# Kernel optimization log

Hardware: AMD Instinct MI355X
Metric: run time of the kernel (lower is better)

Reference implementation:

```python
import jax, jax.numpy as jnp
import numpy as np

B, CIN, COUT = 4, 256, 256
H, W = 48, 48
KH = KW = 7
SH = SW = 1
PH = PW = 3
REL = COUT // 2  # rel_size with groups=1


def setup_inputs() -> dict:
    key = jax.random.key(0)
    ks = jax.random.split(key, 7)
    fan = float(CIN)
    x = jax.random.normal(ks[0], (B, CIN, H, W), jnp.float32)
    w_q = jax.random.normal(ks[1], (COUT, CIN), jnp.float32) * (2.0 / fan) ** 0.5
    w_k = jax.random.normal(ks[2], (COUT, CIN), jnp.float32) * (2.0 / fan) ** 0.5
    w_v = jax.random.normal(ks[3], (COUT, CIN), jnp.float32) * (2.0 / fan) ** 0.5
    bound = 1.0 / np.sqrt(COUT)
    bias = jax.random.uniform(ks[4], (1, COUT, 1, 1), jnp.float32, -bound, bound)
    rel_x = jax.random.normal(ks[5], (REL, KW), jnp.float32)
    rel_y = jax.random.normal(ks[6], (COUT - REL, KH), jnp.float32)
    return {"x": x, "w_q": w_q, "w_k": w_k, "w_v": w_v, "bias": bias,
            "rel_x": rel_x, "rel_y": rel_y}


def reference(x, w_q, w_k, w_v, bias, rel_x, rel_y):
    b = x.shape[0]
    ph, pw = H + 2 * PH, W + 2 * PW
    fh = (ph - KH) // SH + 1
    fw = (pw - KW) // SW + 1
    xp = jnp.pad(x, ((0, 0), (0, 0), (PH, PH), (PW, PW)))
    # 1x1 convs (groups=1) as channel matmuls
    vq = jnp.einsum('oc,bchw->bohw', w_q, xp)
    vk = jnp.einsum('oc,bchw->bohw', w_k, xp)
    vv = jnp.einsum('oc,bchw->bohw', w_v, xp)
    # query at window centers: [b, C, fh, fw]
    win_q = vq[:, :, (KH - 1) // 2: ph - KH // 2: SH, (KW - 1) // 2: pw - KW // 2: SW]
    # relative position terms (sum over channel halves)
    qx = jnp.einsum('bxhw,xk->bhwk', win_q[:, :REL], rel_x)        # [b,fh,fw,kw]
    qy = jnp.einsum('byhw,yk->bhwk', win_q[:, REL:], rel_y)        # [b,fh,fw,kh]
    # overlapping windows via gather (equivalent to torch unfold)
    I = jnp.arange(fh)[:, None] * SH + jnp.arange(KH)[None, :]     # [fh,kh]
    J = jnp.arange(fw)[:, None] * SW + jnp.arange(KW)[None, :]     # [fw,kw]
    win_k = vk[:, :, I[:, None, :, None], J[None, :, None, :]]     # [b,C,fh,fw,kh,kw]
    # channel-summed attention logits (shared across channels, as in source)
    scores = jnp.einsum('bchw,bchwkl->bhwkl', win_q, win_k)
    scores = scores + qy[:, :, :, :, None] + qx[:, :, :, None, :]
    attn = jax.nn.softmax(scores.reshape(b, fh, fw, KH * KW), axis=-1)
    attn = attn.reshape(b, fh, fw, KH, KW)
    win_v = vv[:, :, I[:, None, :, None], J[None, :, None, :]]     # [b,C,fh,fw,kh,kw]
    out = jnp.einsum('bhwkl,bchwkl->bchw', attn, win_v) + bias
    return out
```

## Files before the change

### kernel.cpp

```cpp
#include <hip/hip_runtime.h>

#define BB 4
#define CC 256
#define HH 48
#define WW 48
#define HWHW 2304
#define KK 49
#define RELN 128

#define QSZ (BB*CC*HWHW)
#define ATTNOFF (3*QSZ)
#define SBUF_FLOATS (BB*HH*64*WW)
#define WTOFF (ATTNOFF + SBUF_FLOATS)
#define WT_FLOATS 196608
#define KBOFF (WTOFF + WT_FLOATS)
#define KB_FLOATS 3145728
#define RBOFF (KBOFF + KB_FLOATS)

typedef short bf16x8 __attribute__((ext_vector_type(8)));
typedef float f32x4 __attribute__((ext_vector_type(4)));

__device__ __forceinline__ void split_bf16(float f, unsigned short& hi, unsigned short& lo)
{
    unsigned u = __float_as_uint(f);
    hi = (unsigned short)(u >> 16);
    float r = f - __uint_as_float(u & 0xFFFF0000u);
    unsigned v = __float_as_uint(r);
    v += 0x7FFFu + ((v >> 16) & 1u);
    lo = (unsigned short)(v >> 16);
}

__device__ __forceinline__ void gload16(const uint4* g, uint4* l)
{
    __builtin_amdgcn_global_load_lds(
        (const __attribute__((address_space(1))) void*)g,
        (__attribute__((address_space(3))) void*)l, 16, 0, 0);
}

__global__ __launch_bounds__(256) void prep_kernel(
    const float* __restrict__ x,
    const float* __restrict__ wq, const float* __restrict__ wk,
    const float* __restrict__ wvp,
    const float* __restrict__ relx, const float* __restrict__ rely,
    unsigned short* __restrict__ xt, unsigned short* __restrict__ wt,
    float* __restrict__ ws)
{
    __shared__ unsigned short lds[32*520];
    const int bid = blockIdx.x;
    const int t = threadIdx.x;

    if (bid < 288) {
        const int b = bid / 72;
        const int hw0 = (bid % 72) * 32;
        const int hw = t & 31, cp = t >> 5;
        #pragma unroll 4
        for (int i = 0; i < 32; ++i) {
            int c = i*8 + cp;
            float f = x[((size_t)b*CC + c)*HWHW + hw0 + hw];
            unsigned short hi, lo; split_bf16(f, hi, lo);
            int ch = i*2;
            lds[hw*520 + ((ch       ^ (hw&7))*8) + cp] = hi;
            lds[hw*520 + (((ch + 1) ^ (hw&7))*8) + cp] = lo;
        }
        __syncthreads();
        const int hw2 = t >> 3, u = t & 7;
        uint4* xt4 = (uint4*)xt;
        const size_t rowbase = ((size_t)b*HWHW + hw0 + hw2) * 64;
        #pragma unroll
        for (int j = 0; j < 8; ++j) {
            int chunk = j*8 + u;
            uint4 v = *(const uint4*)&lds[hw2*520 + chunk*8];
            xt4[rowbase + chunk] = v;
        }
        return;
    }
    if (bid < 384) {
        const int tt = (bid - 288)*256 + t;
        const int m = tt >> 5, kg = tt & 31;
        const float* src = (m < 256) ? wq : (m < 512) ? wk : wvp;
        const float* row = src + (size_t)(m & 255)*256 + kg*8;
        unsigned short h[8], l[8];
        #pragma unroll
        for (int j = 0; j < 8; ++j) split_bf16(row[j], h[j], l[j]);
        uint4 hv, lv;
        hv.x = (unsigned)h[0] | ((unsigned)h[1]<<16); hv.y = (unsigned)h[2] | ((unsigned)h[3]<<16);
        hv.z = (unsigned)h[4] | ((unsigned)h[5]<<16); hv.w = (unsigned)h[6] | ((unsigned)h[7]<<16);
        lv.x = (unsigned)l[0] | ((unsigned)l[1]<<16); lv.y = (unsigned)l[2] | ((unsigned)l[3]<<16);
        lv.z = (unsigned)l[4] | ((unsigned)l[5]<<16); lv.w = (unsigned)l[6] | ((unsigned)l[7]<<16);
        uint4* dstrow = (uint4*)wt + (size_t)m*64;
        const int ks = kg >> 2, s_hi = 2*(kg & 3);
        dstrow[ks*8 + ( s_hi      ^ (m&7))] = hv;
        dstrow[ks*8 + ((s_hi + 1) ^ (m&7))] = lv;
        return;
    }
    if (bid < 576) {
        uint4* kb4 = (uint4*)(ws + KBOFF);
        const uint4 z = make_uint4(0u,0u,0u,0u);
        int u0 = (bid - 384)*256 + t;
        #pragma unroll
        for (int it = 0; it < 4; ++it) {
            int u = u0 + it*49152;
            int bch = u >> 7, rem = u & 127;
            int r16 = rem >> 3, gr = rem & 7;
            int r = (r16 < 3) ? r16 : 48 + r16;
            kb4[((size_t)bch*64 + r)*8 + gr] = z;
        }
        return;
    }
    {
        unsigned short* rb = (unsigned short*)(ws + RBOFF);
        #pragma unroll
        for (int it = 0; it < 4; ++it) {
            int idx = t + it*256;
            int gi  = idx & 7;
            int l   = (idx >> 3) & 15;
            int ck4 = (idx >> 7) & 3;
            int rel = idx >> 9;
            int isLo = gi >> 2, g4i = gi & 3;
            unsigned short vals[8];
            #pragma unroll
            for (int j = 0; j < 8; ++j) {
                int cl = ck4*32 + g4i*8 + j;
                float f = (l < 7) ? (rel ? rely[cl*7 + l] : relx[cl*7 + l]) : 0.f;
                unsigned short hi, lo; split_bf16(f, hi, lo);
                vals[j] = isLo ? lo : hi;
            }
            int slot = gi ^ (l & 7);
            unsigned short* dst = rb + (((size_t)rel*4 + ck4)*16 + l)*64 + slot*8;
            uint4 pack;
            pack.x = (unsigned)vals[0] | ((unsigned)vals[1]<<16);
            pack.y = (unsigned)vals[2] | ((unsigned)vals[3]<<16);
            pack.z = (unsigned)vals[4] | ((unsigned)vals[5]<<16);
            pack.w = (unsigned)vals[6] | ((unsigned)vals[7]<<16);
            *(uint4*)dst = pack;
        }
    }
}

__global__ __launch_bounds__(512) void proj_gemm_kernel(
    const unsigned short* __restrict__ xt,
    const unsigned short* __restrict__ wt,
    float* __restrict__ ws)
{
    __shared__ uint4 smem[2][2560];
    const int m0 = blockIdx.x * 256;
    const int n0 = blockIdx.y * 64;
    const int b = n0 / HWHW;
    const int hwb = n0 % HWHW;
    const int tid = threadIdx.x;
    const int wid = tid >> 6, ln = tid & 63;
    const int wm = wid >> 1, wn = wid & 1;
    const int l15 = ln & 15, g = ln >> 4;

    f32x4 acc[4][2];
    #pragma unroll
    for (int i = 0; i < 4; ++i)
        #pragma unroll
        for (int j = 0; j < 2; ++j) acc[i][j] = (f32x4){0.f,0.f,0.f,0.f};

    const uint4* wt4 = (const uint4*)wt;
    const uint4* xt4 = (const uint4*)xt;
    const int lrow = ln >> 3, lslot = ln & 7;

    #define STAGE(bf, ks)                                                          \
        {                                                                          \
            _Pragma("unroll")                                                      \
            for (int i = 0; i < 4; ++i) {                                          \
                int seg = wid*4 + i;                                               \
                int row = seg*8 + lrow;                                            \
                gload16(wt4 + (size_t)(m0 + row)*64 + (ks)*8 + lslot,              \
                        &smem[bf][seg*64]);                                        \
            }                                                                      \
            {                                                                      \
                int row = wid*8 + lrow;                                            \
                gload16(xt4 + (size_t)(n0 + row)*64 + (ks)*8 + lslot,              \
                        &smem[bf][2048 + wid*64]);                                 \
            }                                                                      \
        }

    STAGE(0, 0);
    #pragma unroll
    for (int ks = 0; ks < 8; ++ks) {
        const int cur = ks & 1;
        if (ks < 7) STAGE(cur ^ 1, ks + 1);
        if (ks < 7) asm volatile("s_waitcnt vmcnt(5)" ::: "memory");
        else        asm volatile("s_waitcnt vmcnt(0)" ::: "memory");
        __builtin_amdgcn_s_barrier();
        __builtin_amdgcn_sched_barrier(0);
        bf16x8 aH[4], aL[4], bH[2], bL[2];
        #pragma unroll
        for (int mt = 0; mt < 4; ++mt) {
            int rA = wm*64 + mt*16 + l15;
            aH[mt] = *(const bf16x8*)&smem[cur][rA*8 + ((2*g)   ^ (rA&7))];
            aL[mt] = *(const bf16x8*)&smem[cur][rA*8 + ((2*g+1) ^ (rA&7))];
        }
        #pragma unroll
        for (int nt = 0; nt < 2; ++nt) {
            int rB = wn*32 + nt*16 + l15;
            bH[nt] = *(const bf16x8*)&smem[cur][2048 + rB*8 + ((2*g)   ^ (rB&7))];
            bL[nt] = *(const bf16x8*)&smem[cur][2048 + rB*8 + ((2*g+1) ^ (rB&7))];
        }
        #pragma unroll
        for (int mt = 0; mt < 4; ++mt)
            #pragma unroll
            for (int nt = 0; nt < 2; ++nt) {
                acc[mt][nt] = __builtin_amdgcn_mfma_f32_16x16x32_bf16(aH[mt], bH[nt], acc[mt][nt], 0, 0, 0);
                acc[mt][nt] = __builtin_amdgcn_mfma_f32_16x16x32_bf16(aH[mt], bL[nt], acc[mt][nt], 0, 0, 0);
                acc[mt][nt] = __builtin_amdgcn_mfma_f32_16x16x32_bf16(aL[mt], bH[nt], acc[mt][nt], 0, 0, 0);
            }
        if (ks < 7) {
            asm volatile("s_waitcnt lgkmcnt(0)" ::: "memory");
            __builtin_amdgcn_s_barrier();
        }
    }
    #undef STAGE

    const int proj = blockIdx.x;
    if (proj == 2) {
        #pragma unroll
        for (int mt = 0; mt < 4; ++mt) {
            int ch4 = wm*16 + mt*4 + g;
            #pragma unroll
            for (int nt = 0; nt < 2; ++nt) {
                int hw = hwb + wn*32 + nt*16 + l15;
                float* dst = ws + (size_t)2*QSZ + (((size_t)b*64 + ch4)*HWHW + hw)*4;
                *(f32x4*)dst = acc[mt][nt];
            }
        }
        return;
    }
    __syncthreads();
    unsigned short* eb = (unsigned short*)&smem[0][0];
    #pragma unroll
    for (int mt = 0; mt < 4; ++mt) {
        const int chb = wm*64 + mt*16 + 4*g;
        const int ck = chb >> 5;
        const int p = chb & 31, g8 = p >> 3, half = (p >> 2) & 1;
        #pragma unroll
        for (int nt = 0; nt < 2; ++nt) {
            const int hwl = wn*32 + nt*16 + l15;
            const int w = (hwb + hwl) % 48;
            const int key = (proj == 0 ? w : w + 3) & 7;
            f32x4 v = acc[mt][nt];
            unsigned short h0,h1,h2,h3,q0,q1,q2,q3;
            split_bf16(v[0],h0,q0); split_bf16(v[1],h1,q1);
            split_bf16(v[2],h2,q2); split_bf16(v[3],h3,q3);
            uint2 hv, lv;
            hv.x = (unsigned)h0 | ((unsigned)h1<<16); hv.y = (unsigned)h2 | ((unsigned)h3<<16);
            lv.x = (unsigned)q0 | ((unsigned)q1<<16); lv.y = (unsigned)q2 | ((unsigned)q3<<16);
            const int base = (ck*64 + hwl)*64;
            *(uint2*)(eb + base + ((g8 ^ key)*8 + half*4))     = hv;
            *(uint2*)(eb + base + (((g8+4) ^ key)*8 + half*4)) = lv;
        }
    }
    __syncthreads();
    if (proj == 0) {
        const uint4* src = (const uint4*)eb;
        uint4* qb4 = (uint4*)ws;
        #pragma unroll
        for (int ck = 0; ck < 8; ++ck) {
            uint4* dst = qb4 + (((size_t)b*8 + ck)*HWHW + hwb)*8;
            dst[tid] = src[ck*512 + tid];
        }
    } else {
        uint4* kb4 = (uint4*)(ws + KBOFF);
        const uint4* src = (const uint4*)eb;
        #pragma unroll
        for (int it = 0; it < 8; ++it) {
            int u = it*512 + tid;
            int row = u >> 3, gr = u & 7;
            int ck = row >> 6, hwl = row & 63;
            int hw2 = hwb + hwl, h2 = hw2/48, w2 = hw2%48;
            kb4[((((size_t)b*8 + ck)*48 + h2)*64 + (w2+3))*8 + gr] = src[u];
        }
    }
}

__global__ __launch_bounds__(512) void scores2_kernel(float* __restrict__ ws)
{
    __shared__ unsigned short sAll[2][4096*8];
    __shared__ float sc[63][48];

    const int bid = blockIdx.x;
    const int b = bid / 48, h = bid % 48;
    const int tid = threadIdx.x;
    const int wv = tid >> 6, ln = tid & 63;
    const int l15 = ln & 15, g4 = ln >> 4;
    const int key = l15 & 7;

    const unsigned short* QB = (const unsigned short*)ws;
    const unsigned short* KB = (const unsigned short*)(ws + KBOFF);
    const unsigned short* RB = (const unsigned short*)(ws + RBOFF);

    for (int u = tid; u < 63*48; u += 512) ((float*)sc)[u] = 0.f;

    const int dk = wv;
    const int hp = h + dk - 3;
    const bool dok = (wv < 7) && (hp >= 0) && (hp < 48);

    f32x4 acc[6], qx[3], qy[3];
    #pragma unroll
    for (int i = 0; i < 6; ++i) acc[i] = (f32x4){0.f,0.f,0.f,0.f};
    #pragma unroll
    for (int i = 0; i < 3; ++i) { qx[i] = (f32x4){0.f,0.f,0.f,0.f}; qy[i] = (f32x4){0.f,0.f,0.f,0.f}; }

    #define SSTAGE(bf, ck)                                                         \
        {                                                                          \
            _Pragma("unroll")                                                      \
            for (int e = 0; e < 8; ++e) {                                          \
                const int I = wv*8 + e;                                            \
                uint4* dst = (uint4*)sAll[bf] + I*64;                              \
                if (I < 6) {                                                       \
                    int unit = I*64 + ln; int row = unit >> 3, gr = unit & 7;      \
                    gload16((const uint4*)QB                                       \
                        + ((((size_t)b*8 + (ck))*48 + h)*48 + row)*8 + gr, dst);   \
                } else if (I < 62) {                                               \
                    int uk = (I-6)*64 + ln;                                        \
                    int kri = uk >> 9;                                             \
                    int wi = uk & 511; int row = wi >> 3, gr = wi & 7;             \
                    int kh = h + kri - 3;                                          \
                    int khc = kh < 0 ? 0 : (kh > 47 ? 47 : kh);                    \
                    gload16((const uint4*)KB                                       \
                        + ((((size_t)b*8 + (ck))*48 + khc)*64 + row)*8 + gr, dst); \
                } else {                                                           \
                    int ur = (I-62)*64 + ln; int row = ur >> 3, gr = ur & 7;       \
                    int rel = (ck) >> 2, c4 = (ck) & 3;                            \
                    gload16((const uint4*)RB                                       \
                        + (((size_t)rel*4 + c4)*16 + row)*8 + gr, dst);            \
                }                                                                  \
            }                                                                      \
        }

    SSTAGE(0, 0);
    for (int ck = 0; ck < 8; ++ck) {
        const int cur = ck & 1;
        if (ck < 7) SSTAGE(cur ^ 1, ck + 1);
        if (ck < 7) asm volatile("s_waitcnt vmcnt(8)" ::: "memory");
        else        asm volatile("s_waitcnt vmcnt(0)" ::: "memory");
        __builtin_amdgcn_s_barrier();
        __builtin_amdgcn_sched_barrier(0);

        const unsigned short* sQ = sAll[cur];
        const unsigned short* sK = sAll[cur] + 384*8;
        const unsigned short* sR = sAll[cur] + 3968*8;

        bf16x8 AH[3], AL[3];
        #pragma unroll
        for (int i = 0; i < 3; ++i) {
            const unsigned short* qr = sQ + (16*i + l15)*64;
            AH[i] = *(const bf16x8*)(qr + ((g4       ^ key)*8));
            AL[i] = *(const bf16x8*)(qr + (((g4 + 4) ^ key)*8));
        }

        if (wv < 7) {
            if (dok) {
                const unsigned short* kbase = sK + dk*4096;
                bf16x8 BH[4], BL[4];
                #pragma unroll
                for (int j = 0; j < 4; ++j) {
                    const unsigned short* kr = kbase + (j*16 + l15)*64;
                    BH[j] = *(const bf16x8*)(kr + ((g4       ^ key)*8));
                    BL[j] = *(const bf16x8*)(kr + (((g4 + 4) ^ key)*8));
                }
                #pragma unroll
                for (int i = 0; i < 3; ++i) {
                    acc[i*2]   = __builtin_amdgcn_mfma_f32_16x16x32_bf16(AH[i], BH[i],   acc[i*2],   0,0,0);
                    acc[i*2]   = __builtin_amdgcn_mfma_f32_16x16x32_bf16(AH[i], BL[i],   acc[i*2],   0,0,0);
                    acc[i*2]   = __builtin_amdgcn_mfma_f32_16x16x32_bf16(AL[i], BH[i],   acc[i*2],   0,0,0);
                    acc[i*2+1] = __builtin_amdgcn_mfma_f32_16x16x32_bf16(AH[i], BH[i+1], acc[i*2+1], 0,0,0);
                    acc[i*2+1] = __builtin_amdgcn_mfma_f32_16x16x32_bf16(AH[i], BL[i+1], acc[i*2+1], 0,0,0);
                    acc[i*2+1] = __builtin_amdgcn_mfma_f32_16x16x32_bf16(AL[i], BH[i+1], acc[i*2+1], 0,0,0);
                }
            }
        } else {
            const unsigned short* rr = sR + l15*64;
            bf16x8 RH = *(const bf16x8*)(rr + ((g4       ^ key)*8));
            bf16x8 RL = *(const bf16x8*)(rr + (((g4 + 4) ^ key)*8));
            if (ck < 4) {
                #pragma unroll
                for (int i = 0; i < 3; ++i) {
                    qx[i] = __builtin_amdgcn_mfma_f32_16x16x32_bf16(AH[i], RH, qx[i], 0,0,0);
                    qx[i] = __builtin_amdgcn_mfma_f32_16x16x32_bf16(AH[i], RL, qx[i], 0,0,0);
                    qx[i] = __builtin_amdgcn_mfma_f32_16x16x32_bf16(AL[i], RH, qx[i], 0,0,0);
                }
            } else {
                #pragma unroll
                for (int i = 0; i < 3; ++i) {
                    qy[i] = __builtin_amdgcn_mfma_f32_16x16x32_bf16(AH[i], RH, qy[i], 0,0,0);
                    qy[i] = __builtin_amdgcn_mfma_f32_16x16x32_bf16(AH[i], RL, qy[i], 0,0,0);
                    qy[i] = __builtin_amdgcn_mfma_f32_16x16x32_bf16(AL[i], RH, qy[i], 0,0,0);
                }
            }
        }
        if (ck < 7) {
            asm volatile("s_waitcnt lgkmcnt(0)" ::: "memory");
            __builtin_amdgcn_s_barrier();
        }
    }
    #undef SSTAGE

    const int n = l15;
    if (wv < 7) {
        if (dok) {
            #pragma unroll
            for (int i = 0; i < 3; ++i)
                #pragma unroll
                for (int a = 0; a < 2; ++a) {
                    f32x4 A = acc[i*2+a];
                    #pragma unroll
                    for (int r = 0; r < 4; ++r) {
                        int m = 4*g4 + r;
                        int dl = n - m + a*16;
                        if (dl >= 0 && dl < 7)
                            sc[dk*7 + dl][16*i + m] = A[r];
                    }
                }
        }
    } else {
        if (n < 7) {
            #pragma unroll
            for (int i = 0; i < 3; ++i)
                #pragma unroll
                for (int r = 0; r < 4; ++r) {
                    sc[49 + n][16*i + 4*g4 + r] = qx[i][r];
                    sc[56 + n][16*i + 4*g4 + r] = qy[i][r];
                }
        }
    }
    __syncthreads();

    if (tid < 48) {
        const int w = tid;
        float tot[KK], rx[7], ry[7];
        #pragma unroll
        for (int i = 0; i < KK; ++i) tot[i] = sc[i][w];
        #pragma unroll
        for (int l = 0; l < 7; ++l) { rx[l] = sc[49+l][w]; ry[l] = sc[56+l][w]; }
        float mx = -1e30f;
        #pragma unroll
        for (int dk2 = 0; dk2 < 7; ++dk2)
            #pragma unroll
            for (int dl = 0; dl < 7; ++dl) {
                tot[dk2*7+dl] += ry[dk2] + rx[dl];
                mx = fmaxf(mx, tot[dk2*7+dl]);
            }
        float sum = 0.f;
        #pragma unroll
        for (int i = 0; i < KK; ++i) { float e = __expf(tot[i]-mx); tot[i]=e; sum += e; }
        float inv = 1.f/sum;
        float* base = ws + ATTNOFF + ((size_t)(b*HH + h)*64)*WW + w;
        #pragma unroll
        for (int i = 0; i < KK; ++i) base[(size_t)i*WW] = tot[i]*inv;
    }
}

__global__ __launch_bounds__(192) void pv_kernel(
    const float* __restrict__ bias,
    const float* __restrict__ ws,
    float* __restrict__ out)
{
    const float* vbuf = ws + (size_t)2*QSZ;
    const float* attn = ws + ATTNOFF;
    __shared__ f32x4 vtile[4*10*56];

    const int bid = blockIdx.x;
    const int cg = bid & 15;
    const int hs = (bid >> 4) % 12;
    const int b  = bid / (16*12);
    const int h0 = hs*4;

    const int t = threadIdx.x;
    const int hl = t / 48, w = t % 48;
    const int h = h0 + hl;

    const float* ab = attn + ((size_t)(b*HH + h)*64)*WW + w;
    float a[KK];
    #pragma unroll
    for (int i = 0; i < KK; ++i) a[i] = ab[(size_t)i*WW];

    for (int s = t; s < 4*10*56; s += 192) {
        int chq = s / 560;
        int rem = s - chq*560;
        int row = rem / 56, wslot = rem - row*56;
        int gr = h0 + row - 3, gc = wslot - 3;
        f32x4 v = (f32x4){0.f,0.f,0.f,0.f};
        if (gr >= 0 && gr < HH && gc >= 0 && gc < WW)
            v = *(const f32x4*)(vbuf + (((size_t)b*64 + cg*4 + chq)*HWHW + gr*WW + gc)*4);
        vtile[s] = v;
    }
    __syncthreads();

    #pragma unroll
    for (int chq = 0; chq < 4; ++chq) {
        const float4 b4 = *(const float4*)(bias + cg*16 + chq*4);
        f32x4 acc = (f32x4){b4.x, b4.y, b4.z, b4.w};
        #pragma unroll
        for (int dk = 0; dk < 7; ++dk) {
            const f32x4* vrow = &vtile[(chq*10 + hl + dk)*56 + w];
            #pragma unroll
            for (int dl = 0; dl < 7; ++dl)
                acc += vrow[dl] * a[dk*7+dl];
        }
        float* ob = out + ((size_t)(b*CC + cg*16 + chq*4))*HWHW + (size_t)h*WW + w;
        #pragma unroll
        for (int c = 0; c < 4; ++c) ob[(size_t)c*HWHW] = acc[c];
    }
}

extern "C" void kernel_launch(void* const* d_in, const int* in_sizes, int n_in,
                              void* d_out, int out_size, void* d_ws, size_t ws_size,
                              hipStream_t stream) {
    const float* x    = (const float*)d_in[0];
    const float* wq   = (const float*)d_in[1];
    const float* wk   = (const float*)d_in[2];
    const float* wv   = (const float*)d_in[3];
    const float* bias = (const float*)d_in[4];
    const float* relx = (const float*)d_in[5];
    const float* rely = (const float*)d_in[6];
    float* ws  = (float*)d_ws;
    float* out = (float*)d_out;
    unsigned short* xt = (unsigned short*)d_out;
    unsigned short* wt = (unsigned short*)(ws + WTOFF);

    prep_kernel<<<dim3(577), dim3(256), 0, stream>>>(x, wq, wk, wv, relx, rely, xt, wt, ws);
    proj_gemm_kernel<<<dim3(3, 144), dim3(512), 0, stream>>>(xt, wt, ws);
    scores2_kernel<<<dim3(BB*HH), dim3(512), 0, stream>>>(ws);
    pv_kernel<<<dim3(BB*12*16), dim3(192), 0, stream>>>(bias, ws, out);
}
```

Measured before the change: 64.52 us.

## Split scores over channel halves with atomic reduction and separate softmax kernel

The scores kernel now launches two blocks per (batch,row), each handling half of the channel chunks with half-width stages. Partial logits and relative-position terms are atomically accumulated into a global scores buffer, which prep_kernel now zeroes. A new softmax kernel then reads that buffer and writes the normalized weights. The split doubles the grid from 192 blocks to improve occupancy and overlap. In exchange it adds float atomics, a zeroing pass, an extra launch and a global round trip for the scores.

```diff
diff --git a/kernel.cpp b/kernel.cpp
--- a/kernel.cpp
+++ b/kernel.cpp
@@ -49,9 +49,15 @@
     const int bid = blockIdx.x;
     const int t = threadIdx.x;
 
-    if (bid < 288) {
-        const int b = bid / 72;
-        const int hw0 = (bid % 72) * 32;
+    if (bid < 576) {
+        f32x4* p = (f32x4*)(ws + ATTNOFF);
+        p[bid*256 + t] = (f32x4){0.f,0.f,0.f,0.f};
+        return;
+    }
+    if (bid < 864) {
+        const int bid2 = bid - 576;
+        const int b = bid2 / 72;
+        const int hw0 = (bid2 % 72) * 32;
         const int hw = t & 31, cp = t >> 5;
         #pragma unroll 4
         for (int i = 0; i < 32; ++i) {
@@ -74,8 +80,8 @@
         }
         return;
     }
-    if (bid < 384) {
-        const int tt = (bid - 288)*256 + t;
+    if (bid < 960) {
+        const int tt = (bid - 864)*256 + t;
         const int m = tt >> 5, kg = tt & 31;
         const float* src = (m < 256) ? wq : (m < 512) ? wk : wvp;
         const float* row = src + (size_t)(m & 255)*256 + kg*8;
@@ -93,10 +99,10 @@
         dstrow[ks*8 + ((s_hi + 1) ^ (m&7))] = lv;
         return;
     }
-    if (bid < 576) {
+    if (bid < 1152) {
         uint4* kb4 = (uint4*)(ws + KBOFF);
         const uint4 z = make_uint4(0u,0u,0u,0u);
-        int u0 = (bid - 384)*256 + t;
+        int u0 = (bid - 960)*256 + t;
         #pragma unroll
         for (int it = 0; it < 4; ++it) {
             int u = u0 + it*49152;
@@ -276,123 +282,124 @@
     }
 }
 
-__global__ __launch_bounds__(512) void scores2_kernel(float* __restrict__ ws)
-{
-    __shared__ unsigned short sAll[2][4096*8];
-    __shared__ float sc[63][48];
+__global__ __launch_bounds__(512) void scores3_kernel(float* __restrict__ ws)
+{
+    __shared__ unsigned short sAll[2][16384];
+    __shared__ uint4 zgu;
 
     const int bid = blockIdx.x;
-    const int b = bid / 48, h = bid % 48;
+    const int ckp = bid & 1;
+    const int h = (bid >> 1) % 48;
+    const int b = bid / 96;
     const int tid = threadIdx.x;
     const int wv = tid >> 6, ln = tid & 63;
     const int l15 = ln & 15, g4 = ln >> 4;
-    const int key = l15 & 7;
-
-    const unsigned short* QB = (const unsigned short*)ws;
-    const unsigned short* KB = (const unsigned short*)(ws + KBOFF);
-    const unsigned short* RB = (const unsigned short*)(ws + RBOFF);
-
-    for (int u = tid; u < 63*48; u += 512) ((float*)sc)[u] = 0.f;
+
+    const uint4* QB4 = (const uint4*)ws;
+    const uint4* KB4 = (const uint4*)(ws + KBOFF);
+    const uint4* RB4 = (const uint4*)(ws + RBOFF);
+    float* sbuf = ws + ATTNOFF + (size_t)(b*HH + h)*64*WW;
+
+    if (tid == 0) zgu = make_uint4(0u,0u,0u,0u);
+    asm volatile("s_waitcnt lgkmcnt(0)" ::: "memory");
 
     const int dk = wv;
     const int hp = h + dk - 3;
     const bool dok = (wv < 7) && (hp >= 0) && (hp < 48);
 
-    f32x4 acc[6], qx[3], qy[3];
+    f32x4 acc[6], qr[3];
     #pragma unroll
     for (int i = 0; i < 6; ++i) acc[i] = (f32x4){0.f,0.f,0.f,0.f};
     #pragma unroll
-    for (int i = 0; i < 3; ++i) { qx[i] = (f32x4){0.f,0.f,0.f,0.f}; qy[i] = (f32x4){0.f,0.f,0.f,0.f}; }
-
-    #define SSTAGE(bf, ck)                                                         \
+    for (int i = 0; i < 3; ++i) qr[i] = (f32x4){0.f,0.f,0.f,0.f};
+
+    const int colc = ln >> 2, sg = ln & 3;
+
+    #define SSTAGE(bf, T)                                                          \
         {                                                                          \
+            const int ht = ckp*8 + (T);                                            \
+            const int ck = ht >> 1, hf = ht & 1;                                   \
             _Pragma("unroll")                                                      \
-            for (int e = 0; e < 8; ++e) {                                          \
-                const int I = wv*8 + e;                                            \
-                uint4* dst = (uint4*)sAll[bf] + I*64;                              \
-                if (I < 6) {                                                       \
-                    int unit = I*64 + ln; int row = unit >> 3, gr = unit & 7;      \
-                    gload16((const uint4*)QB                                       \
-                        + ((((size_t)b*8 + (ck))*48 + h)*48 + row)*8 + gr, dst);   \
-                } else if (I < 62) {                                               \
-                    int uk = (I-6)*64 + ln;                                        \
-                    int kri = uk >> 9;                                             \
-                    int wi = uk & 511; int row = wi >> 3, gr = wi & 7;             \
-                    int kh = h + kri - 3;                                          \
+            for (int e = 0; e < 4; ++e) {                                          \
+                const int I = wv*4 + e;                                            \
+                if (I < 28) {                                                      \
+                    int kr = I >> 2, qt = I & 3;                                   \
+                    int col = qt*16 + colc;                                        \
+                    int gi = sg ^ (col & 3);                                       \
+                    int lg = (gi < 2) ? (2*hf + gi) : (2*hf + gi + 2);             \
+                    int ss = lg ^ (col & 7);                                       \
+                    int kh = h + kr - 3;                                           \
                     int khc = kh < 0 ? 0 : (kh > 47 ? 47 : kh);                    \
-                    gload16((const uint4*)KB                                       \
-                        + ((((size_t)b*8 + (ck))*48 + khc)*64 + row)*8 + gr, dst); \
+                    gload16(KB4 + ((((size_t)b*8 + ck)*48 + khc)*64 + col)*8 + ss, \
+                            (uint4*)&sAll[bf][(kr*64 + qt*16)*32]);                \
+                } else if (I < 31) {                                               \
+                    int u = I - 28;                                                \
+                    int w2 = u*16 + colc;                                          \
+                    int gi = sg ^ (w2 & 3);                                        \
+                    int lg = (gi < 2) ? (2*hf + gi) : (2*hf + gi + 2);             \
+                    int ss = lg ^ (w2 & 7);                                        \
+                    gload16(QB4 + ((((size_t)b*8 + ck)*48 + h)*48 + w2)*8 + ss,    \
+                            (uint4*)&sAll[bf][14336 + u*512]);                     \
                 } else {                                                           \
-                    int ur = (I-62)*64 + ln; int row = ur >> 3, gr = ur & 7;       \
-                    int rel = (ck) >> 2, c4 = (ck) & 3;                            \
-                    gload16((const uint4*)RB                                       \
-                        + (((size_t)rel*4 + c4)*16 + row)*8 + gr, dst);            \
+                    int l = colc & 15;                                             \
+                    int gi = sg ^ (l & 3);                                         \
+                    int lg = (gi < 2) ? (2*hf + gi) : (2*hf + gi + 2);             \
+                    int ss = lg ^ (l & 7);                                         \
+                    int rel = ck >> 2, c4 = ck & 3;                                \
+                    gload16(RB4 + (((size_t)rel*4 + c4)*16 + l)*8 + ss,            \
+                            (uint4*)&sAll[bf][15872]);                             \
                 }                                                                  \
             }                                                                      \
         }
 
     SSTAGE(0, 0);
-    for (int ck = 0; ck < 8; ++ck) {
-        const int cur = ck & 1;
-        if (ck < 7) SSTAGE(cur ^ 1, ck + 1);
-        if (ck < 7) asm volatile("s_waitcnt vmcnt(8)" ::: "memory");
-        else        asm volatile("s_waitcnt vmcnt(0)" ::: "memory");
+    for (int t = 0; t < 8; ++t) {
+        const int cur = t & 1;
+        if (t < 7) SSTAGE(cur ^ 1, t + 1);
+        if (t < 7) asm volatile("s_waitcnt vmcnt(4)" ::: "memory");
+        else       asm volatile("s_waitcnt vmcnt(0)" ::: "memory");
         __builtin_amdgcn_s_barrier();
         __builtin_amdgcn_sched_barrier(0);
 
-        const unsigned short* sQ = sAll[cur];
-        const unsigned short* sK = sAll[cur] + 384*8;
-        const unsigned short* sR = sAll[cur] + 3968*8;
-
-        bf16x8 AH[3], AL[3];
+        const unsigned short* S = sAll[cur];
+
+        bf16x8 AM1[3], AM2[3];
         #pragma unroll
         for (int i = 0; i < 3; ++i) {
-            const unsigned short* qr = sQ + (16*i + l15)*64;
-            AH[i] = *(const bf16x8*)(qr + ((g4       ^ key)*8));
-            AL[i] = *(const bf16x8*)(qr + (((g4 + 4) ^ key)*8));
+            int row = 16*i + l15;
+            AM1[i] = *(const bf16x8*)&S[14336 + row*32 + (((g4&1) ^ (row&3)))*8];
+            AM2[i] = (g4 < 2)
+                ? *(const bf16x8*)&S[14336 + row*32 + (((2+g4) ^ (row&3)))*8]
+                : *(const bf16x8*)&zgu;
         }
 
         if (wv < 7) {
             if (dok) {
-                const unsigned short* kbase = sK + dk*4096;
-                bf16x8 BH[4], BL[4];
+                bf16x8 BM1[4], BM2[4];
                 #pragma unroll
                 for (int j = 0; j < 4; ++j) {
-                    const unsigned short* kr = kbase + (j*16 + l15)*64;
-                    BH[j] = *(const bf16x8*)(kr + ((g4       ^ key)*8));
-                    BL[j] = *(const bf16x8*)(kr + (((g4 + 4) ^ key)*8));
+                    int r = j*16 + l15;
+                    BM1[j] = *(const bf16x8*)&S[dk*2048 + r*32 + ((g4     ^ (r&3)))*8];
+                    BM2[j] = *(const bf16x8*)&S[dk*2048 + r*32 + (((g4&1) ^ (r&3)))*8];
                 }
                 #pragma unroll
                 for (int i = 0; i < 3; ++i) {
-                    acc[i*2]   = __builtin_amdgcn_mfma_f32_16x16x32_bf16(AH[i], BH[i],   acc[i*2],   0,0,0);
-                    acc[i*2]   = __builtin_amdgcn_mfma_f32_16x16x32_bf16(AH[i], BL[i],   acc[i*2],   0,0,0);
-                    acc[i*2]   = __builtin_amdgcn_mfma_f32_16x16x32_bf16(AL[i], BH[i],   acc[i*2],   0,0,0);
-                    acc[i*2+1] = __builtin_amdgcn_mfma_f32_16x16x32_bf16(AH[i], BH[i+1], acc[i*2+1], 0,0,0);
-                    acc[i*2+1] = __builtin_amdgcn_mfma_f32_16x16x32_bf16(AH[i], BL[i+1], acc[i*2+1], 0,0,0);
-                    acc[i*2+1] = __builtin_amdgcn_mfma_f32_16x16x32_bf16(AL[i], BH[i+1], acc[i*2+1], 0,0,0);
+                    acc[i*2]   = __builtin_amdgcn_mfma_f32_16x16x32_bf16(AM1[i], BM1[i],   acc[i*2],   0,0,0);
+                    acc[i*2]   = __builtin_amdgcn_mfma_f32_16x16x32_bf16(AM2[i], BM2[i],   acc[i*2],   0,0,0);
+                    acc[i*2+1] = __builtin_amdgcn_mfma_f32_16x16x32_bf16(AM1[i], BM1[i+1], acc[i*2+1], 0,0,0);
+                    acc[i*2+1] = __builtin_amdgcn_mfma_f32_16x16x32_bf16(AM2[i], BM2[i+1], acc[i*2+1], 0,0,0);
                 }
             }
         } else {
-            const unsigned short* rr = sR + l15*64;
-            bf16x8 RH = *(const bf16x8*)(rr + ((g4       ^ key)*8));
-            bf16x8 RL = *(const bf16x8*)(rr + (((g4 + 4) ^ key)*8));
-            if (ck < 4) {
-                #pragma unroll
-                for (int i = 0; i < 3; ++i) {
-                    qx[i] = __builtin_amdgcn_mfma_f32_16x16x32_bf16(AH[i], RH, qx[i], 0,0,0);
-                    qx[i] = __builtin_amdgcn_mfma_f32_16x16x32_bf16(AH[i], RL, qx[i], 0,0,0);
-                    qx[i] = __builtin_amdgcn_mfma_f32_16x16x32_bf16(AL[i], RH, qx[i], 0,0,0);
-                }
-            } else {
-                #pragma unroll
-                for (int i = 0; i < 3; ++i) {
-                    qy[i] = __builtin_amdgcn_mfma_f32_16x16x32_bf16(AH[i], RH, qy[i], 0,0,0);
-                    qy[i] = __builtin_amdgcn_mfma_f32_16x16x32_bf16(AH[i], RL, qy[i], 0,0,0);
-                    qy[i] = __builtin_amdgcn_mfma_f32_16x16x32_bf16(AL[i], RH, qy[i], 0,0,0);
-                }
+            bf16x8 RM1 = *(const bf16x8*)&S[15872 + l15*32 + ((g4     ^ (l15&3)))*8];
+            bf16x8 RM2 = *(const bf16x8*)&S[15872 + l15*32 + (((g4&1) ^ (l15&3)))*8];
+            #pragma unroll
+            for (int i = 0; i < 3; ++i) {
+                qr[i] = __builtin_amdgcn_mfma_f32_16x16x32_bf16(AM1[i], RM1, qr[i], 0,0,0);
+                qr[i] = __builtin_amdgcn_mfma_f32_16x16x32_bf16(AM2[i], RM2, qr[i], 0,0,0);
             }
         }
-        if (ck < 7) {
+        if (t < 7) {
             asm volatile("s_waitcnt lgkmcnt(0)" ::: "memory");
             __builtin_amdgcn_s_barrier();
         }
@@ -412,46 +419,51 @@
                         int m = 4*g4 + r;
                         int dl = n - m + a*16;
                         if (dl >= 0 && dl < 7)
-                            sc[dk*7 + dl][16*i + m] = A[r];
+                            atomicAdd(sbuf + (size_t)(dk*7 + dl)*WW + (16*i + m), A[r]);
                     }
                 }
         }
     } else {
         if (n < 7) {
+            const int slot0 = ckp ? 56 : 49;
             #pragma unroll
             for (int i = 0; i < 3; ++i)
                 #pragma unroll
-                for (int r = 0; r < 4; ++r) {
-                    sc[49 + n][16*i + 4*g4 + r] = qx[i][r];
-                    sc[56 + n][16*i + 4*g4 + r] = qy[i][r];
-                }
-        }
-    }
-    __syncthreads();
-
-    if (tid < 48) {
-        const int w = tid;
-        float tot[KK], rx[7], ry[7];
-        #pragma unroll
-        for (int i = 0; i < KK; ++i) tot[i] = sc[i][w];
-        #pragma unroll
-        for (int l = 0; l < 7; ++l) { rx[l] = sc[49+l][w]; ry[l] = sc[56+l][w]; }
-        float mx = -1e30f;
-        #pragma unroll
-        for (int dk2 = 0; dk2 < 7; ++dk2)
-            #pragma unroll
-            for (int dl = 0; dl < 7; ++dl) {
-                tot[dk2*7+dl] += ry[dk2] + rx[dl];
-                mx = fmaxf(mx, tot[dk2*7+dl]);
-            }
-        float sum = 0.f;
-        #pragma unroll
-        for (int i = 0; i < KK; ++i) { float e = __expf(tot[i]-mx); tot[i]=e; sum += e; }
-        float inv = 1.f/sum;
-        float* base = ws + ATTNOFF + ((size_t)(b*HH + h)*64)*WW + w;
-        #pragma unroll
-        for (int i = 0; i < KK; ++i) base[(size_t)i*WW] = tot[i]*inv;
-    }
+                for (int r = 0; r < 4; ++r)
+                    atomicAdd(sbuf + (size_t)(slot0 + n)*WW + (16*i + 4*g4 + r), qr[i][r]);
+        }
+    }
+}
+
+__global__ __launch_bounds__(64) void softmax_kernel(float* __restrict__ ws)
+{
+    float* sbuf = ws + ATTNOFF;
+    const int p = blockIdx.x*64 + threadIdx.x;
+    const int w = p % WW;
+    const int bh = p / WW;
+    float* base = sbuf + (size_t)bh*64*WW + w;
+
+    float tot[KK], qx[7], qy[7];
+    #pragma unroll
+    for (int i=0;i<KK;i++) tot[i] = base[(size_t)i*WW];
+    #pragma unroll
+    for (int l=0;l<7;l++) { qx[l] = base[(size_t)(49+l)*WW]; qy[l] = base[(size_t)(56+l)*WW]; }
+
+    float mx = -1e30f;
+    #pragma unroll
+    for (int dk=0;dk<7;dk++) {
+        #pragma unroll
+        for (int dl=0;dl<7;dl++) {
+            tot[dk*7+dl] += qy[dk] + qx[dl];
+            mx = fmaxf(mx, tot[dk*7+dl]);
+        }
+    }
+    float sum = 0.f;
+    #pragma unroll
+    for (int i=0;i<KK;i++) { float e = __expf(tot[i]-mx); tot[i]=e; sum += e; }
+    float inv = 1.f/sum;
+    #pragma unroll
+    for (int i=0;i<KK;i++) base[(size_t)i*WW] = tot[i]*inv;
 }
 
 __global__ __launch_bounds__(192) void pv_kernel(
@@ -522,8 +534,9 @@
     unsigned short* xt = (unsigned short*)d_out;
     unsigned short* wt = (unsigned short*)(ws + WTOFF);
 
-    prep_kernel<<<dim3(577), dim3(256), 0, stream>>>(x, wq, wk, wv, relx, rely, xt, wt, ws);
+    prep_kernel<<<dim3(1153), dim3(256), 0, stream>>>(x, wq, wk, wv, relx, rely, xt, wt, ws);
     proj_gemm_kernel<<<dim3(3, 144), dim3(512), 0, stream>>>(xt, wt, ws);
-    scores2_kernel<<<dim3(BB*HH), dim3(512), 0, stream>>>(ws);
+    scores3_kernel<<<dim3(BB*HH*2), dim3(512), 0, stream>>>(ws);
+    softmax_kernel<<<dim3(144), dim3(64), 0, stream>>>(ws);
     pv_kernel<<<dim3(BB*12*16), dim3(192), 0, stream>>>(bias, ws, out);
 }
```

Measured after the change: 79.99 us. +24.0%, slower.
